# Optimization experiments

Hardware: AMD Instinct MI355X
Metric: run time of the kernel (lower is better)

Reference implementation:

```python
import jax, jax.numpy as jnp
import numpy as np

PI = float(np.pi)


def _layernorm(x, g, b, eps=1e-5):
    mu = jnp.mean(x, axis=-1, keepdims=True)
    var = jnp.var(x, axis=-1, keepdims=True)
    return (x - mu) * jax.lax.rsqrt(var + eps) * g + b


def setup_inputs() -> dict:
    key = jax.random.key(0)
    B, L, D, P = 4, 2048, 256, 32
    ks = jax.random.split(key, 16)

    def lin_w(k, fi, fo):
        return (jax.random.normal(k, (fi, fo), dtype=jnp.float32) / np.sqrt(fi)).astype(jnp.float32)

    inp = {
        'x': jax.random.normal(ks[0], (B, L, D), dtype=jnp.float32),
        'pos_phases': jax.random.normal(ks[1], (L, P), dtype=jnp.float32) * PI,
        'w_mem1v': lin_w(ks[2], D, P), 'b_mem1v': jnp.zeros((P,), jnp.float32),
        'w_mem1o': lin_w(ks[3], P, D), 'b_mem1o': jnp.zeros((D,), jnp.float32),
        'w_off': lin_w(ks[4], D + P, P), 'b_off': jnp.zeros((P,), jnp.float32),
        'w_key': lin_w(ks[5], D, P), 'b_key': jnp.zeros((P,), jnp.float32),
        'w_val': lin_w(ks[6], D, D), 'b_val': jnp.zeros((D,), jnp.float32),
        'w_sk1': lin_w(ks[7], 2 * D, D), 'b_sk1': jnp.zeros((D,), jnp.float32),
        'w_sk2': lin_w(ks[8], D, P), 'b_sk2': jnp.zeros((P,), jnp.float32),
        'w_gate': lin_w(ks[9], D, 1), 'b_gate': jnp.zeros((1,), jnp.float32),
        'ln_g': jnp.ones((D,), jnp.float32), 'ln_b': jnp.zeros((D,), jnp.float32),
        'w_out': lin_w(ks[10], D, D), 'b_out': jnp.zeros((D,), jnp.float32),
    }
    return inp


def reference(x, pos_phases, w_mem1v, b_mem1v, w_mem1o, b_mem1o, w_off, b_off,
              w_key, b_key, w_val, b_val, w_sk1, b_sk1, w_sk2, b_sk2,
              w_gate, b_gate, ln_g, ln_b, w_out, b_out):
    B, L, D = x.shape
    P = pos_phases.shape[-1]

    pos_cos = jnp.cos(pos_phases)  # [L,P]
    pos_sin = jnp.sin(pos_phases)

    # Memory 1: flat [B,L,P] phasor cumulative memory
    v1 = x @ w_mem1v + b_mem1v                       # [B,L,P]
    mem1_cos = jnp.cumsum(pos_cos[None] * v1, axis=1)
    mem1_sin = jnp.cumsum(pos_sin[None] * v1, axis=1)

    offset_input = jnp.concatenate([x, jnp.broadcast_to(pos_phases[None], (B, L, P))], axis=-1)
    offset = jnp.tanh(offset_input @ w_off + b_off) * PI
    oc, os = jnp.cos(offset), jnp.sin(offset)
    query_cos = pos_cos[None] * oc - pos_sin[None] * os
    query_sin = pos_sin[None] * oc + pos_cos[None] * os
    pos_ret = (mem1_cos * query_cos + mem1_sin * query_sin) / np.sqrt(P)
    pos_out = pos_ret @ w_mem1o + b_mem1o            # [B,L,D]

    # Memory 2: full [B,L,P,D] phasor KV cumulative memory
    key_phases = jnp.tanh(x @ w_key + b_key) * PI    # [B,L,P]
    key_cos, key_sin = jnp.cos(key_phases), jnp.sin(key_phases)
    values = x @ w_val + b_val                       # [B,L,D]
    store_gate = jax.nn.sigmoid(x @ w_gate + b_gate) # [B,L,1]

    positions = jnp.arange(1, L + 1, dtype=x.dtype)[None, :, None]
    context_avg = jnp.cumsum(x, axis=1) / positions
    h = jax.nn.gelu(jnp.concatenate([x, context_avg], axis=-1) @ w_sk1 + b_sk1, approximate=False)
    storage_phases = jnp.tanh(h @ w_sk2 + b_sk2) * PI  # [B,L,P]

    gated_v = values * store_gate                    # [B,L,D]
    kv_mem_cos = jnp.cumsum(jnp.cos(storage_phases)[..., None] * gated_v[:, :, None, :], axis=1)  # [B,L,P,D]
    kv_mem_sin = jnp.cumsum(jnp.sin(storage_phases)[..., None] * gated_v[:, :, None, :], axis=1)

    gate_cumsum = jnp.clip(jnp.cumsum(store_gate, axis=1), 1.0, None)  # [B,L,1]
    kv_retrieved = jnp.einsum('blpd,blp->bld', kv_mem_cos, key_cos) + \
                   jnp.einsum('blpd,blp->bld', kv_mem_sin, key_sin)
    kv_retrieved = kv_retrieved / (jnp.sqrt(gate_cumsum) * np.sqrt(P))

    combined = pos_out + kv_retrieved
    return x + _layernorm(combined, ln_g, ln_b) @ w_out + b_out
```

## Files before the change

kernel.cpp:

```cpp
#include <hip/hip_runtime.h>
#include <hip/hip_bf16.h>

constexpr int B_ = 4;
constexpr int L_ = 2048;
constexpr int D_ = 256;
constexpr int P_ = 32;
constexpr int CL = 32;
constexpr int NC = L_ / CL;

#define PI_F 3.14159265358979323846f
#define INV_SQRT_P 0.17677669529663687f

typedef __attribute__((ext_vector_type(8))) short short8_t;
typedef __attribute__((ext_vector_type(4))) float floatx4;

static __device__ inline short f2bf(float f) {
  unsigned int u;
  __builtin_memcpy(&u, &f, 4);
  unsigned int r = (u + 0x7fffu + ((u >> 16) & 1u)) >> 16;
  return (short)r;
}
static __device__ inline float bf2f(short s) {
  unsigned int u = ((unsigned int)(unsigned short)s) << 16;
  float f;
  __builtin_memcpy(&f, &u, 4);
  return f;
}

__global__ void wprep(const float* __restrict__ x, const float* __restrict__ pos,
                      const float* __restrict__ w_val, const float* __restrict__ w_mem1v,
                      const float* __restrict__ w_off, const float* __restrict__ b_off,
                      const float* __restrict__ w_key, const float* __restrict__ w_gate,
                      const float* __restrict__ w_sk1, const float* __restrict__ w_out,
                      const float* __restrict__ w_sk2, const float* __restrict__ w_mem1o,
                      short* __restrict__ WA, short* __restrict__ W1,
                      short* __restrict__ WO, short* __restrict__ W2T,
                      short* __restrict__ W1OT,
                      short* __restrict__ xbf, float* __restrict__ poff,
                      float* __restrict__ ctxsum) {
  __shared__ float2 psum[2][128];
  int blk = blockIdx.x, tid = threadIdx.x;
  if (blk < 384) {
    int idx = blk * 256 + tid;
    int n = idx >> 8, k = idx & 255;
    float v;
    if (n < 256) v = w_val[k * 256 + n];
    else if (n < 288) v = w_mem1v[k * 32 + (n - 256)];
    else if (n < 320) v = w_off[k * 32 + (n - 288)];
    else if (n < 352) v = w_key[k * 32 + (n - 320)];
    else if (n == 352) v = w_gate[k];
    else v = 0.f;
    WA[idx] = f2bf(v);
  } else if (blk < 896) {
    int idx = (blk - 384) * 256 + tid;
    int n = idx >> 9, k = idx & 511;
    W1[idx] = f2bf(w_sk1[k * 256 + n]);
  } else if (blk < 1152) {
    int idx = (blk - 896) * 256 + tid;
    int n = idx >> 8, k = idx & 255;
    WO[idx] = f2bf(w_out[k * 256 + n]);
  } else if (blk < 1184) {
    int idx = (blk - 1152) * 256 + tid;
    int p = idx >> 8, k = idx & 255;
    W2T[idx] = f2bf(w_sk2[k * 32 + p]);
  } else if (blk < 1216) {
    int idx = (blk - 1184) * 256 + tid;
    int d = idx >> 5, p = idx & 31;
    W1OT[idx] = f2bf(w_mem1o[p * 256 + d]);
  } else if (blk < 1472) {
    int idx = (blk - 1216) * 256 + tid;
    int l = idx >> 5, p = idx & 31;
    float a = b_off[p];
#pragma unroll 8
    for (int j = 0; j < 32; ++j) a += pos[l * 32 + j] * w_off[(256 + j) * 32 + p];
    poff[idx] = a;
  } else {
    int c2 = blk - 1472;
    int b = c2 >> 6, ch = c2 & 63;
    int d2 = (tid & 127) * 2, h = tid >> 7;
    int tokb = b * L_ + ch * 32 + h * 16;
    float2 xv[16];
#pragma unroll
    for (int i = 0; i < 16; ++i)
      xv[i] = *(const float2*)&x[(tokb + i) * 256 + d2];
    float2 s = {0.f, 0.f};
#pragma unroll
    for (int i = 0; i < 16; ++i) { s.x += xv[i].x; s.y += xv[i].y; }
#pragma unroll
    for (int i = 0; i < 16; ++i) {
      short2 o;
      o.x = f2bf(xv[i].x);
      o.y = f2bf(xv[i].y);
      *(short2*)&xbf[(tokb + i) * 256 + d2] = o;
    }
    psum[h][tid & 127] = s;
    __syncthreads();
    if (h == 0) {
      float2 o = psum[1][tid & 127];
      float2 tot = {s.x + o.x, s.y + o.y};
      *(float2*)&ctxsum[c2 * 256 + d2] = tot;
    }
  }
}

__global__ __launch_bounds__(768, 6) void gemmA3(const short* __restrict__ xbf,
                                                 const short* __restrict__ WA,
                                                 const float* __restrict__ pos,
                                                 const float* __restrict__ poff,
                                                 const float* __restrict__ b_mem1v,
                                                 const float* __restrict__ b_key,
                                                 const float* __restrict__ b_gate,
                                                 const float* __restrict__ b_val,
                                                 float* __restrict__ m1cT,
                                                 float* __restrict__ m1sT,
                                                 float* __restrict__ qc,
                                                 float* __restrict__ qs,
                                                 short* __restrict__ K2bf,
                                                 short* __restrict__ gvT,
                                                 float* __restrict__ sg,
                                                 float* __restrict__ ctxsum) {
  __shared__ float YL[16][132];
  __shared__ float gsh[16];
  int tid = threadIdx.x;
  int bc = blockIdx.x;
  if (bc >= 512) {
    if (tid < 256) {
      int b = bc - 512;
      int base = b * 64 * 256 + tid;
      float run = 0.f;
      for (int c0 = 0; c0 < 64; c0 += 8) {
        float v[8];
#pragma unroll
        for (int j = 0; j < 8; ++j) v[j] = ctxsum[base + (c0 + j) * 256];
#pragma unroll
        for (int j = 0; j < 8; ++j) {
          ctxsum[base + (c0 + j) * 256] = run;
          run += v[j];
        }
      }
    }
    return;
  }
  int lane = tid & 63, w = tid >> 6;
  int ml = lane & 15, quad = lane >> 4, kq = quad * 8;
  int bc32 = bc >> 1, half = bc & 1;
  int tok0 = bc * 16;
  floatx4 acc[2] = {};
  const short* A0p = &xbf[(tok0 + ml) * 256 + kq];
  const short* Bp = &WA[(w * 32 + ml) * 256 + kq];
#pragma unroll
  for (int ks = 0; ks < 8; ++ks) {
    short8_t a0 = *(const short8_t*)(A0p + ks * 32);
#pragma unroll
    for (int nt = 0; nt < 2; ++nt) {
      short8_t b = *(const short8_t*)(Bp + nt * 16 * 256 + ks * 32);
      acc[nt] = __builtin_amdgcn_mfma_f32_16x16x32_bf16(a0, b, acc[nt], 0, 0, 0);
    }
  }
  if (w >= 8) {
#pragma unroll
    for (int nt = 0; nt < 2; ++nt) {
      int col = (w - 8) * 32 + nt * 16 + ml;
#pragma unroll
      for (int r = 0; r < 4; ++r)
        YL[quad * 4 + r][col] = acc[nt][r];
    }
  }
  __syncthreads();
  if (tid < 512) {
    int t = tid >> 5, p = tid & 31;
    int tok = tok0 + t, l = tok & (L_ - 1);
    int b = tok >> 11;
    float v1 = YL[t][p] + b_mem1v[p];
    float ph = pos[l * 32 + p];
    float pc = cosf(ph), ps = sinf(ph);
    int idxT = (b * 32 + p) * L_ + l;
    m1cT[idxT] = pc * v1;
    m1sT[idxT] = ps * v1;
    float off = tanhf(YL[t][32 + p] + poff[l * 32 + p]) * PI_F;
    float oc = cosf(off), os = sinf(off);
    int gidx = tok * 32 + p;
    qc[gidx] = pc * oc - ps * os;
    qs[gidx] = ps * oc + pc * os;
    float kp = tanhf(YL[t][64 + p] + b_key[p]) * PI_F;
    K2bf[tok * 64 + p] = f2bf(cosf(kp));
    K2bf[tok * 64 + 32 + p] = f2bf(sinf(kp));
    if (p == 0) {
      float g = 1.f / (1.f + expf(-(YL[t][96] + b_gate[0])));
      sg[tok] = g;
      gsh[t] = g;
    }
  }
  __syncthreads();
  if (w < 8) {
#pragma unroll
    for (int nt = 0; nt < 2; ++nt) {
      int d = w * 32 + nt * 16 + ml;
      float bv = b_val[d];
      int t0 = quad * 4;
      short4 o;
      o.x = f2bf((acc[nt][0] + bv) * gsh[t0 + 0]);
      o.y = f2bf((acc[nt][1] + bv) * gsh[t0 + 1]);
      o.z = f2bf((acc[nt][2] + bv) * gsh[t0 + 2]);
      o.w = f2bf((acc[nt][3] + bv) * gsh[t0 + 3]);
      *(short4*)&gvT[(bc32 * 256 + d) * 32 + half * 16 + t0] = o;
    }
  }
}

union __align__(16) CDMem {
  short As[32][520];
  struct { short HS[32][280]; short SPL[64][40]; } h;
};
__global__ __launch_bounds__(1024, 4) void gemmCD(const short* __restrict__ xbf,
                                                  const float* __restrict__ x,
                                                  const float* __restrict__ ctxsum,
                                                  const short* __restrict__ W1,
                                                  const float* __restrict__ b_sk1,
                                                  const short* __restrict__ W2T,
                                                  const float* __restrict__ b_sk2,
                                                  const short* __restrict__ gvT,
                                                  short* __restrict__ SPbf,
                                                  short* __restrict__ UT) {
  __shared__ CDMem sm;
  __shared__ float stmp[4][256];
  int tid = threadIdx.x;
  int bc = blockIdx.x;
  int tok0 = bc * 32;
  int bI = bc >> 6, ch = bc & 63;
  int lane = tid & 63, w = tid >> 6;
  int ml = lane & 15, quad = lane >> 4, kq = quad * 8;
  {
    int row = tid >> 5, c8 = tid & 31;
    *(short8_t*)&sm.As[row][c8 * 8] =
        *(const short8_t*)&xbf[(tok0 + row) * 256 + c8 * 8];
  }
  {
    int d = tid & 255, qh = tid >> 8;
    float cp = ctxsum[(bI * 64 + ch) * 256 + d];
    float xv[8];
    int xb = (tok0 + qh * 8) * 256 + d;
#pragma unroll
    for (int i = 0; i < 8; ++i) xv[i] = x[xb + i * 256];
    float p = 0.f;
#pragma unroll
    for (int i = 0; i < 8; ++i) p += xv[i];
    stmp[qh][d] = p;
    __syncthreads();
    float run = cp;
    for (int j = 0; j < qh; ++j) run += stmp[j][d];
    int l0 = ch * 32 + qh * 8;
#pragma unroll
    for (int i = 0; i < 8; ++i) {
      run += xv[i];
      sm.As[qh * 8 + i][256 + d] = f2bf(run / (float)(l0 + i + 1));
    }
  }
  __syncthreads();
  int n0w = w * 16;
  floatx4 acc[2] = {};
#pragma unroll
  for (int kt = 0; kt < 16; ++kt) {
    short8_t a0 = *(short8_t*)&sm.As[ml][kt * 32 + kq];
    short8_t a1 = *(short8_t*)&sm.As[16 + ml][kt * 32 + kq];
    short8_t b0 = *(const short8_t*)&W1[(n0w + ml) * 512 + kt * 32 + kq];
    acc[0] = __builtin_amdgcn_mfma_f32_16x16x32_bf16(a0, b0, acc[0], 0, 0, 0);
    acc[1] = __builtin_amdgcn_mfma_f32_16x16x32_bf16(a1, b0, acc[1], 0, 0, 0);
  }
  short hv[2][4];
  {
    float bv = b_sk1[n0w + ml];
#pragma unroll
    for (int mt = 0; mt < 2; ++mt)
#pragma unroll
      for (int r = 0; r < 4; ++r) {
        float v = acc[mt][r] + bv;
        float g = 0.5f * v * (1.f + erff(v * 0.70710678118654752f));
        hv[mt][r] = f2bf(g);
      }
  }
  __syncthreads();
#pragma unroll
  for (int mt = 0; mt < 2; ++mt)
#pragma unroll
    for (int r = 0; r < 4; ++r)
      sm.h.HS[mt * 16 + quad * 4 + r][n0w + ml] = hv[mt][r];
  __syncthreads();
  if (w < 4) {
    int th = w & 1, ph = w >> 1;
    floatx4 pacc = {};
#pragma unroll
    for (int s = 0; s < 8; ++s) {
      short8_t a = *(short8_t*)&sm.h.HS[th * 16 + ml][s * 32 + kq];
      short8_t b0 = *(const short8_t*)&W2T[(ph * 16 + ml) * 256 + s * 32 + kq];
      pacc = __builtin_amdgcn_mfma_f32_16x16x32_bf16(a, b0, pacc, 0, 0, 0);
    }
    int p = ph * 16 + ml;
    float bs = b_sk2[p];
#pragma unroll
    for (int r = 0; r < 4; ++r) {
      int tl = th * 16 + quad * 4 + r;
      int tok = tok0 + tl;
      float sp = tanhf(pacc[r] + bs) * PI_F;
      short c = f2bf(cosf(sp)), s2 = f2bf(sinf(sp));
      sm.h.SPL[p][tl] = c;
      sm.h.SPL[32 + p][tl] = s2;
      SPbf[tok * 64 + p] = c;
      SPbf[tok * 64 + 32 + p] = s2;
    }
  }
  __syncthreads();
  short8_t a[4];
#pragma unroll
  for (int mt = 0; mt < 4; ++mt) a[mt] = *(short8_t*)&sm.h.SPL[mt * 16 + ml][kq];
  floatx4 acc3[4] = {};
  {
    int d = w * 16 + ml;
    short8_t b = *(const short8_t*)&gvT[(bc * 256 + d) * 32 + kq];
#pragma unroll
    for (int mt = 0; mt < 4; ++mt)
      acc3[mt] = __builtin_amdgcn_mfma_f32_16x16x32_bf16(a[mt], b, acc3[mt], 0, 0, 0);
  }
#pragma unroll
  for (int mt = 0; mt < 4; ++mt) {
    int d = w * 16 + ml;
    short4 o;
    o.x = f2bf(acc3[mt][0]);
    o.y = f2bf(acc3[mt][1]);
    o.z = f2bf(acc3[mt][2]);
    o.w = f2bf(acc3[mt][3]);
    *(short4*)&UT[(bc * 256 + d) * 64 + mt * 16 + quad * 4] = o;
  }
}

__global__ void scanE(float* __restrict__ m1cT, float* __restrict__ m1sT,
                      float* __restrict__ sg, short* __restrict__ UT) {
  int blk = blockIdx.x;
  int tid = threadIdx.x;
  if (blk >= 260) {
    int t = (blk - 260) * 256 + tid;
    int pi = t >> 2, j = t & 3;
    int q = pi & 63;
    int d = (pi >> 6) & 255;
    int b = pi >> 14;
    const int cs = 256 * 64;
    int base = ((b * NC) * 256 + d) * 64 + q + j * 16 * cs;
    short v[16];
#pragma unroll
    for (int c = 0; c < 16; ++c) v[c] = UT[base + c * cs];
    float tot = 0.f;
#pragma unroll
    for (int c = 0; c < 16; ++c) tot += bf2f(v[c]);
    int lane = tid & 63;
    int gb = lane & ~3;
    float t0 = __shfl(tot, gb + 0, 64);
    float t1 = __shfl(tot, gb + 1, 64);
    float t2 = __shfl(tot, gb + 2, 64);
    float run = (j > 0 ? t0 : 0.f) + (j > 1 ? t1 : 0.f) + (j > 2 ? t2 : 0.f);
#pragma unroll
    for (int c = 0; c < 16; ++c) {
      UT[base + c * cs] = f2bf(run);
      run += bf2f(v[c]);
    }
    return;
  }
  __shared__ float wsum[4];
  int lane = tid & 63, w = tid >> 6;
  float* arr;
  int base;
  if (blk < 256) {
    arr = (blk < 128) ? m1cT : m1sT;
    base = (blk & 127) * L_;
  } else {
    arr = sg;
    base = (blk - 256) * L_;
  }
  int sbase = base + w * 512;
  float v[8];
#pragma unroll
  for (int i = 0; i < 8; ++i) v[i] = arr[sbase + i * 64 + lane];
  float carry = 0.f;
#pragma unroll
  for (int i = 0; i < 8; ++i) {
    float vv = v[i];
#pragma unroll
    for (int off = 1; off < 64; off <<= 1) {
      float n = __shfl_up(vv, off, 64);
      if (lane >= off) vv += n;
    }
    vv += carry;
    v[i] = vv;
    carry = __shfl(vv, 63, 64);
  }
  if (lane == 0) wsum[w] = carry;
  __syncthreads();
  float off = 0.f;
  for (int ww = 0; ww < w; ++ww) off += wsum[ww];
#pragma unroll
  for (int i = 0; i < 8; ++i) arr[sbase + i * 64 + lane] = v[i] + off;
}

struct __align__(16) FGMem {
  short SL[32][40];
  short PR[32][40];
  float CMB[32][260];
  short CBN[32][280];
  float LG[256], LB[256];
  float scl[32], mu_s[32], rs_s[32];
};
__global__ __launch_bounds__(1024, 4) void fgOut(const short* __restrict__ UT,
                                                 const short* __restrict__ SPbf,
                                                 const short* __restrict__ K2bf,
                                                 const short* __restrict__ gvT,
                                                 const float* __restrict__ sgc,
                                                 const float* __restrict__ m1cT,
                                                 const float* __restrict__ m1sT,
                                                 const float* __restrict__ qc,
                                                 const float* __restrict__ qs,
                                                 const short* __restrict__ W1OT,
                                                 const float* __restrict__ b_mem1o,
                                                 const float* __restrict__ ln_g,
                                                 const float* __restrict__ ln_b,
                                                 const short* __restrict__ WO,
                                                 const float* __restrict__ b_out,
                                                 const float* __restrict__ x,
                                                 float* __restrict__ out) {
  __shared__ FGMem sm;
  int tid5 = threadIdx.x;
  int bc = blockIdx.x;
  int lbase = bc * CL;
  int bb = bc >> 6, lloc = (bc & 63) * 32;
  int lane = tid5 & 63, w = tid5 >> 6;
  int ml = lane & 15, quad = lane >> 4, kq = quad * 8;
  int d0 = w * 16;
  if (tid5 < 32) sm.scl[tid5] = rsqrtf(fmaxf(sgc[lbase + tid5], 1.f)) * INV_SQRT_P;
  if (tid5 >= 256 && tid5 < 512) {
    int d = tid5 - 256;
    sm.LG[d] = ln_g[d];
    sm.LB[d] = ln_b[d];
  }
  short8_t ka0 = *(const short8_t*)&K2bf[(lbase + ml) * 64 + kq];
  short8_t ka1 = *(const short8_t*)&K2bf[(lbase + 16 + ml) * 64 + kq];
  short8_t kb0 = *(const short8_t*)&K2bf[(lbase + ml) * 64 + 32 + kq];
  short8_t kb1 = *(const short8_t*)&K2bf[(lbase + 16 + ml) * 64 + 32 + kq];
  if (w == 0) {
    floatx4 sacc[2][2] = {};
#pragma unroll
    for (int ks2 = 0; ks2 < 2; ++ks2) {
      short8_t a0 = (ks2 == 0) ? ka0 : kb0;
      short8_t a1 = (ks2 == 0) ? ka1 : kb1;
      short8_t b0 = *(const short8_t*)&SPbf[(lbase + ml) * 64 + ks2 * 32 + kq];
      short8_t b1 = *(const short8_t*)&SPbf[(lbase + 16 + ml) * 64 + ks2 * 32 + kq];
      sacc[0][0] = __builtin_amdgcn_mfma_f32_16x16x32_bf16(a0, b0, sacc[0][0], 0, 0, 0);
      sacc[0][1] = __builtin_amdgcn_mfma_f32_16x16x32_bf16(a0, b1, sacc[0][1], 0, 0, 0);
      sacc[1][0] = __builtin_amdgcn_mfma_f32_16x16x32_bf16(a1, b0, sacc[1][0], 0, 0, 0);
      sacc[1][1] = __builtin_amdgcn_mfma_f32_16x16x32_bf16(a1, b1, sacc[1][1], 0, 0, 0);
    }
#pragma unroll
    for (int mt = 0; mt < 2; ++mt)
#pragma unroll
      for (int nt = 0; nt < 2; ++nt)
#pragma unroll
        for (int r = 0; r < 4; ++r) {
          int trow = mt * 16 + quad * 4 + r;
          int scol = nt * 16 + ml;
          float v = (scol <= trow) ? sacc[mt][nt][r] : 0.f;
          sm.SL[trow][scol] = f2bf(v);
        }
  } else {
    int t7 = tid5 - 64;
    for (int i = t7; i < 1024; i += 960) {
      int pp = i >> 5, t = i & 31;
      int gT = (bb * 32 + pp) * L_ + lloc + t;
      int g = (lbase + t) * 32 + pp;
      sm.PR[t][pp] = f2bf((m1cT[gT] * qc[g] + m1sT[gT] * qs[g]) * INV_SQRT_P);
    }
  }
  __syncthreads();
  floatx4 acc[2] = {};
  {
    short8_t b0 = *(const short8_t*)&UT[(bc * 256 + d0 + ml) * 64 + kq];
    short8_t b1 = *(const short8_t*)&UT[(bc * 256 + d0 + ml) * 64 + 32 + kq];
    acc[0] = __builtin_amdgcn_mfma_f32_16x16x32_bf16(ka0, b0, acc[0], 0, 0, 0);
    acc[1] = __builtin_amdgcn_mfma_f32_16x16x32_bf16(ka1, b0, acc[1], 0, 0, 0);
    acc[0] = __builtin_amdgcn_mfma_f32_16x16x32_bf16(kb0, b1, acc[0], 0, 0, 0);
    acc[1] = __builtin_amdgcn_mfma_f32_16x16x32_bf16(kb1, b1, acc[1], 0, 0, 0);
  }
  {
    short8_t a0 = *(short8_t*)&sm.SL[ml][kq];
    short8_t a1 = *(short8_t*)&sm.SL[16 + ml][kq];
    short8_t b = *(const short8_t*)&gvT[(bc * 256 + d0 + ml) * 32 + kq];
    acc[0] = __builtin_amdgcn_mfma_f32_16x16x32_bf16(a0, b, acc[0], 0, 0, 0);
    acc[1] = __builtin_amdgcn_mfma_f32_16x16x32_bf16(a1, b, acc[1], 0, 0, 0);
  }
  floatx4 macc[2] = {};
  {
    short8_t a0 = *(short8_t*)&sm.PR[ml][kq];
    short8_t a1 = *(short8_t*)&sm.PR[16 + ml][kq];
    short8_t b = *(const short8_t*)&W1OT[(d0 + ml) * 32 + kq];
    macc[0] = __builtin_amdgcn_mfma_f32_16x16x32_bf16(a0, b, macc[0], 0, 0, 0);
    macc[1] = __builtin_amdgcn_mfma_f32_16x16x32_bf16(a1, b, macc[1], 0, 0, 0);
  }
  {
    int d = d0 + ml;
    float bm = b_mem1o[d];
#pragma unroll
    for (int mt = 0; mt < 2; ++mt)
#pragma unroll
      for (int r = 0; r < 4; ++r) {
        int t = mt * 16 + quad * 4 + r;
        sm.CMB[t][d] = acc[mt][r] * sm.scl[t] + macc[mt][r] + bm;
      }
  }
  __syncthreads();
  {
    int t = tid5 >> 5, g = tid5 & 31;
    float s = 0.f, s2 = 0.f;
#pragma unroll
    for (int j = 0; j < 8; ++j) {
      float v = sm.CMB[t][g + j * 32];
      s += v;
      s2 += v * v;
    }
#pragma unroll
    for (int m = 1; m < 32; m <<= 1) {
      s += __shfl_xor(s, m, 64);
      s2 += __shfl_xor(s2, m, 64);
    }
    if (g == 0) {
      float mu = s / (float)D_;
      float var = s2 / (float)D_ - mu * mu;
      sm.mu_s[t] = mu;
      sm.rs_s[t] = rsqrtf(var + 1e-5f);
    }
  }
  __syncthreads();
#pragma unroll
  for (int it = 0; it < 8; ++it) {
    int i = it * 1024 + tid5;
    int t = i >> 8, d = i & 255;
    sm.CBN[t][d] = f2bf((sm.CMB[t][d] - sm.mu_s[t]) * sm.rs_s[t] * sm.LG[d] + sm.LB[d]);
  }
  __syncthreads();
  floatx4 acc2[2] = {};
#pragma unroll
  for (int kt = 0; kt < 8; ++kt) {
    short8_t a0 = *(short8_t*)&sm.CBN[ml][kt * 32 + kq];
    short8_t a1 = *(short8_t*)&sm.CBN[16 + ml][kt * 32 + kq];
    short8_t b = *(const short8_t*)&WO[(d0 + ml) * 256 + kt * 32 + kq];
    acc2[0] = __builtin_amdgcn_mfma_f32_16x16x32_bf16(a0, b, acc2[0], 0, 0, 0);
    acc2[1] = __builtin_amdgcn_mfma_f32_16x16x32_bf16(a1, b, acc2[1], 0, 0, 0);
  }
  {
    int n = d0 + ml;
    float bv = b_out[n];
#pragma unroll
    for (int mt = 0; mt < 2; ++mt)
#pragma unroll
      for (int r = 0; r < 4; ++r) {
        int tok = lbase + mt * 16 + quad * 4 + r;
        out[tok * 256 + n] = x[tok * 256 + n] + acc2[mt][r] + bv;
      }
  }
}

extern "C" void kernel_launch(void* const* d_in, const int* in_sizes, int n_in,
                              void* d_out, int out_size, void* d_ws, size_t ws_size,
                              hipStream_t stream) {
  const float* x = (const float*)d_in[0];
  const float* pos = (const float*)d_in[1];
  const float* w_mem1v = (const float*)d_in[2];
  const float* b_mem1v = (const float*)d_in[3];
  const float* w_mem1o = (const float*)d_in[4];
  const float* b_mem1o = (const float*)d_in[5];
  const float* w_off = (const float*)d_in[6];
  const float* b_off = (const float*)d_in[7];
  const float* w_key = (const float*)d_in[8];
  const float* b_key = (const float*)d_in[9];
  const float* w_val = (const float*)d_in[10];
  const float* b_val = (const float*)d_in[11];
  const float* w_sk1 = (const float*)d_in[12];
  const float* b_sk1 = (const float*)d_in[13];
  const float* w_sk2 = (const float*)d_in[14];
  const float* b_sk2 = (const float*)d_in[15];
  const float* w_gate = (const float*)d_in[16];
  const float* b_gate = (const float*)d_in[17];
  const float* ln_g = (const float*)d_in[18];
  const float* ln_b = (const float*)d_in[19];
  const float* w_out = (const float*)d_in[20];
  const float* b_out = (const float*)d_in[21];
  float* out = (float*)d_out;
  float* ws = (float*)d_ws;

  const int BLP = B_ * L_ * P_;
  const int BLD = B_ * L_ * D_;
  float* m1cT = ws;
  float* m1sT = m1cT + BLP;
  float* qc = m1sT + BLP;
  float* qs = qc + BLP;
  float* sg = qs + BLP;
  float* poff = sg + B_ * L_;
  float* ctxsum = poff + L_ * P_;
  short* UT = (short*)(ctxsum + B_ * 64 * 256);
  short* xbf = UT + (size_t)B_ * NC * 256 * 64;
  short* ctxbf = xbf + BLD;
  short* hs = ctxbf + BLD;
  short* gvT = hs + BLD;
  short* K2bf = gvT + BLD;
  short* SPbf = K2bf + B_ * L_ * 64;
  short* WA = SPbf + B_ * L_ * 64;
  short* W1 = WA + 384 * 256;
  short* WO = W1 + 256 * 512;
  short* W2T = WO + 256 * 256;
  short* W1OT = W2T + 32 * 256;

  wprep<<<1728, 256, 0, stream>>>(x, pos, w_val, w_mem1v, w_off, b_off, w_key, w_gate,
                                  w_sk1, w_out, w_sk2, w_mem1o, WA, W1, WO, W2T, W1OT,
                                  xbf, poff, ctxsum);
  gemmA3<<<516, 768, 0, stream>>>(xbf, WA, pos, poff, b_mem1v, b_key, b_gate, b_val,
                                  m1cT, m1sT, qc, qs, K2bf, gvT, sg, ctxsum);
  gemmCD<<<256, 1024, 0, stream>>>(xbf, x, ctxsum, W1, b_sk1, W2T, b_sk2, gvT, SPbf, UT);
  scanE<<<1284, 256, 0, stream>>>(m1cT, m1sT, sg, UT);
  fgOut<<<256, 1024, 0, stream>>>(UT, SPbf, K2bf, gvT, sg, m1cT, m1sT, qc, qs,
                                  W1OT, b_mem1o, ln_g, ln_b, WO, b_out, x, out);
}
```

Measured before the change: 162.7 us.

## Prefetch global operands early, restructure UT scan, and vectorize residual output stores

Global loads of pos/poff, the gvT, UT and W1OT MFMA operands, and the residual x tile are hoisted to kernel entry so their latency overlaps earlier GEMM and LDS work. The chunk-offset scan over UT now gives each lane a whole column across four warps, combining partial totals through shared memory instead of lane shuffles. The final kernel stages output in LDS and writes out = x + result with coalesced float4 stores instead of scattered scalar stores. In exchange there is more register pressure from the early-held operands, plus an extra barrier and LDS round trip.

Result: no change. 160.7 us (median of 2 runs) (-1.3%).

```diff
diff --git a/kernel.cpp b/kernel.cpp
--- a/kernel.cpp
+++ b/kernel.cpp
@@ -145,6 +145,13 @@
   int ml = lane & 15, quad = lane >> 4, kq = quad * 8;
   int bc32 = bc >> 1, half = bc & 1;
   int tok0 = bc * 16;
+  float posv = 0.f, poffv = 0.f;
+  if (tid < 512) {
+    int t = tid >> 5, p = tid & 31;
+    int l = (tok0 + t) & (L_ - 1);
+    posv = pos[l * 32 + p];
+    poffv = poff[l * 32 + p];
+  }
   floatx4 acc[2] = {};
   const short* A0p = &xbf[(tok0 + ml) * 256 + kq];
   const short* Bp = &WA[(w * 32 + ml) * 256 + kq];
@@ -172,12 +179,11 @@
     int tok = tok0 + t, l = tok & (L_ - 1);
     int b = tok >> 11;
     float v1 = YL[t][p] + b_mem1v[p];
-    float ph = pos[l * 32 + p];
-    float pc = cosf(ph), ps = sinf(ph);
+    float pc = cosf(posv), ps = sinf(posv);
     int idxT = (b * 32 + p) * L_ + l;
     m1cT[idxT] = pc * v1;
     m1sT[idxT] = ps * v1;
-    float off = tanhf(YL[t][32 + p] + poff[l * 32 + p]) * PI_F;
+    float off = tanhf(YL[t][32 + p] + poffv) * PI_F;
     float oc = cosf(off), os = sinf(off);
     int gidx = tok * 32 + p;
     qc[gidx] = pc * oc - ps * os;
@@ -230,6 +236,7 @@
   int bI = bc >> 6, ch = bc & 63;
   int lane = tid & 63, w = tid >> 6;
   int ml = lane & 15, quad = lane >> 4, kq = quad * 8;
+  short8_t bgv = *(const short8_t*)&gvT[(bc * 256 + w * 16 + ml) * 32 + kq];
   {
     int row = tid >> 5, c8 = tid & 31;
     *(short8_t*)&sm.As[row][c8 * 8] =
@@ -314,13 +321,9 @@
 #pragma unroll
   for (int mt = 0; mt < 4; ++mt) a[mt] = *(short8_t*)&sm.h.SPL[mt * 16 + ml][kq];
   floatx4 acc3[4] = {};
-  {
-    int d = w * 16 + ml;
-    short8_t b = *(const short8_t*)&gvT[(bc * 256 + d) * 32 + kq];
-#pragma unroll
-    for (int mt = 0; mt < 4; ++mt)
-      acc3[mt] = __builtin_amdgcn_mfma_f32_16x16x32_bf16(a[mt], b, acc3[mt], 0, 0, 0);
-  }
+#pragma unroll
+  for (int mt = 0; mt < 4; ++mt)
+    acc3[mt] = __builtin_amdgcn_mfma_f32_16x16x32_bf16(a[mt], bgv, acc3[mt], 0, 0, 0);
 #pragma unroll
   for (int mt = 0; mt < 4; ++mt) {
     int d = w * 16 + ml;
@@ -335,36 +338,36 @@
 
 __global__ void scanE(float* __restrict__ m1cT, float* __restrict__ m1sT,
                       float* __restrict__ sg, short* __restrict__ UT) {
+  __shared__ float wsum[4];
+  __shared__ float stot[4][64];
   int blk = blockIdx.x;
   int tid = threadIdx.x;
   if (blk >= 260) {
-    int t = (blk - 260) * 256 + tid;
-    int pi = t >> 2, j = t & 3;
+    int eb = blk - 260;
+    int w = tid >> 6, lane = tid & 63;
+    int pi = eb * 64 + lane;
     int q = pi & 63;
     int d = (pi >> 6) & 255;
     int b = pi >> 14;
     const int cs = 256 * 64;
-    int base = ((b * NC) * 256 + d) * 64 + q + j * 16 * cs;
+    int base = ((b * NC) * 256 + d) * 64 + q;
     short v[16];
 #pragma unroll
-    for (int c = 0; c < 16; ++c) v[c] = UT[base + c * cs];
+    for (int c = 0; c < 16; ++c) v[c] = UT[base + (w * 16 + c) * cs];
     float tot = 0.f;
 #pragma unroll
     for (int c = 0; c < 16; ++c) tot += bf2f(v[c]);
-    int lane = tid & 63;
-    int gb = lane & ~3;
-    float t0 = __shfl(tot, gb + 0, 64);
-    float t1 = __shfl(tot, gb + 1, 64);
-    float t2 = __shfl(tot, gb + 2, 64);
-    float run = (j > 0 ? t0 : 0.f) + (j > 1 ? t1 : 0.f) + (j > 2 ? t2 : 0.f);
+    stot[w][lane] = tot;
+    __syncthreads();
+    float run = 0.f;
+    for (int ww = 0; ww < w; ++ww) run += stot[ww][lane];
 #pragma unroll
     for (int c = 0; c < 16; ++c) {
-      UT[base + c * cs] = f2bf(run);
+      UT[base + (w * 16 + c) * cs] = f2bf(run);
       run += bf2f(v[c]);
     }
     return;
   }
-  __shared__ float wsum[4];
   int lane = tid & 63, w = tid >> 6;
   float* arr;
   int base;
@@ -433,6 +436,13 @@
   int lane = tid5 & 63, w = tid5 >> 6;
   int ml = lane & 15, quad = lane >> 4, kq = quad * 8;
   int d0 = w * 16;
+  short8_t ub0 = *(const short8_t*)&UT[(bc * 256 + d0 + ml) * 64 + kq];
+  short8_t ub1 = *(const short8_t*)&UT[(bc * 256 + d0 + ml) * 64 + 32 + kq];
+  short8_t gvb = *(const short8_t*)&gvT[(bc * 256 + d0 + ml) * 32 + kq];
+  short8_t w1b = *(const short8_t*)&W1OT[(d0 + ml) * 32 + kq];
+  const float4* x4 = (const float4*)&x[lbase * 256];
+  float4 xp0 = x4[tid5];
+  float4 xp1 = x4[tid5 + 1024];
   if (tid5 < 32) sm.scl[tid5] = rsqrtf(fmaxf(sgc[lbase + tid5], 1.f)) * INV_SQRT_P;
   if (tid5 >= 256 && tid5 < 512) {
     int d = tid5 - 256;
@@ -478,28 +488,22 @@
   }
   __syncthreads();
   floatx4 acc[2] = {};
-  {
-    short8_t b0 = *(const short8_t*)&UT[(bc * 256 + d0 + ml) * 64 + kq];
-    short8_t b1 = *(const short8_t*)&UT[(bc * 256 + d0 + ml) * 64 + 32 + kq];
-    acc[0] = __builtin_amdgcn_mfma_f32_16x16x32_bf16(ka0, b0, acc[0], 0, 0, 0);
-    acc[1] = __builtin_amdgcn_mfma_f32_16x16x32_bf16(ka1, b0, acc[1], 0, 0, 0);
-    acc[0] = __builtin_amdgcn_mfma_f32_16x16x32_bf16(kb0, b1, acc[0], 0, 0, 0);
-    acc[1] = __builtin_amdgcn_mfma_f32_16x16x32_bf16(kb1, b1, acc[1], 0, 0, 0);
-  }
+  acc[0] = __builtin_amdgcn_mfma_f32_16x16x32_bf16(ka0, ub0, acc[0], 0, 0, 0);
+  acc[1] = __builtin_amdgcn_mfma_f32_16x16x32_bf16(ka1, ub0, acc[1], 0, 0, 0);
+  acc[0] = __builtin_amdgcn_mfma_f32_16x16x32_bf16(kb0, ub1, acc[0], 0, 0, 0);
+  acc[1] = __builtin_amdgcn_mfma_f32_16x16x32_bf16(kb1, ub1, acc[1], 0, 0, 0);
   {
     short8_t a0 = *(short8_t*)&sm.SL[ml][kq];
     short8_t a1 = *(short8_t*)&sm.SL[16 + ml][kq];
-    short8_t b = *(const short8_t*)&gvT[(bc * 256 + d0 + ml) * 32 + kq];
-    acc[0] = __builtin_amdgcn_mfma_f32_16x16x32_bf16(a0, b, acc[0], 0, 0, 0);
-    acc[1] = __builtin_amdgcn_mfma_f32_16x16x32_bf16(a1, b, acc[1], 0, 0, 0);
+    acc[0] = __builtin_amdgcn_mfma_f32_16x16x32_bf16(a0, gvb, acc[0], 0, 0, 0);
+    acc[1] = __builtin_amdgcn_mfma_f32_16x16x32_bf16(a1, gvb, acc[1], 0, 0, 0);
   }
   floatx4 macc[2] = {};
   {
     short8_t a0 = *(short8_t*)&sm.PR[ml][kq];
     short8_t a1 = *(short8_t*)&sm.PR[16 + ml][kq];
-    short8_t b = *(const short8_t*)&W1OT[(d0 + ml) * 32 + kq];
-    macc[0] = __builtin_amdgcn_mfma_f32_16x16x32_bf16(a0, b, macc[0], 0, 0, 0);
-    macc[1] = __builtin_amdgcn_mfma_f32_16x16x32_bf16(a1, b, macc[1], 0, 0, 0);
+    macc[0] = __builtin_amdgcn_mfma_f32_16x16x32_bf16(a0, w1b, macc[0], 0, 0, 0);
+    macc[1] = __builtin_amdgcn_mfma_f32_16x16x32_bf16(a1, w1b, macc[1], 0, 0, 0);
   }
   {
     int d = d0 + ml;
@@ -558,9 +562,25 @@
     for (int mt = 0; mt < 2; ++mt)
 #pragma unroll
       for (int r = 0; r < 4; ++r) {
-        int tok = lbase + mt * 16 + quad * 4 + r;
-        out[tok * 256 + n] = x[tok * 256 + n] + acc2[mt][r] + bv;
+        int t = mt * 16 + quad * 4 + r;
+        sm.CMB[t][n] = acc2[mt][r] + bv;
       }
+  }
+  __syncthreads();
+  {
+    float4* o4 = (float4*)&out[lbase * 256];
+#pragma unroll
+    for (int k = 0; k < 2; ++k) {
+      int idx4 = tid5 + k * 1024;
+      int t = idx4 >> 6, dd = (idx4 & 63) * 4;
+      float4 xp = (k == 0) ? xp0 : xp1;
+      float4 o;
+      o.x = xp.x + sm.CMB[t][dd + 0];
+      o.y = xp.y + sm.CMB[t][dd + 1];
+      o.z = xp.z + sm.CMB[t][dd + 2];
+      o.w = xp.w + sm.CMB[t][dd + 3];
+      o4[idx4] = o;
+    }
   }
 }
 
```
